# Kernel tuning notes

Measured on AMD Instinct MI355X. Metric: run time of the kernel, lower is better.

The kernel has to match this reference:

```python
import jax, jax.numpy as jnp
import numpy as np

NUM_HEADS = 16
NUM_KV_HEADS = 4
ROPE_THETA = 10000.0


def apply_rope(x, position_ids, theta):
    # x: [B, S, h, d]; position_ids: [B, S]
    d = x.shape[-1]
    freqs = 1.0 / theta ** (jnp.arange(0, d, 2, dtype=jnp.float32) / d)  # [d/2]
    angles = position_ids.astype(jnp.float32)[..., None] * freqs          # [B, S, d/2]
    cos = jnp.cos(angles)[:, :, None, :]                                  # [B, S, 1, d/2]
    sin = jnp.sin(angles)[:, :, None, :]
    xr = x.astype(jnp.float32).reshape(*x.shape[:-1], d // 2, 2)
    x0, x1 = xr[..., 0], xr[..., 1]
    o0 = x0 * cos - x1 * sin
    o1 = x0 * sin + x1 * cos
    out = jnp.stack((o0, o1), axis=-1).reshape(*x.shape)
    return out.astype(x.dtype)


def setup_inputs() -> dict:
    key = jax.random.key(0)
    k0, k1, k2, k3, k4 = jax.random.split(key, 5)
    B, S, H = 1, 2048, 2048
    Hkv = H // (NUM_HEADS // NUM_KV_HEADS)  # 512
    init_scale = 0.02 / np.sqrt(H)
    return {
        "hidden_states": jax.random.normal(k0, (B, S, H), jnp.float32),
        "attention_mask": jnp.ones((B, S), jnp.int32),
        "segment_ids": jnp.zeros((B, S), jnp.int32),
        "position_ids": jnp.broadcast_to(jnp.arange(S, dtype=jnp.int32)[None], (B, S)),
        "Wq": jax.random.normal(k1, (H, H), jnp.float32) * init_scale,
        "Wk": jax.random.normal(k2, (H, Hkv), jnp.float32) * init_scale,
        "Wv": jax.random.normal(k3, (H, Hkv), jnp.float32) * init_scale,
        "Wo": jax.random.normal(k4, (H, H), jnp.float32) * init_scale,
    }


def reference(hidden_states, attention_mask, segment_ids, position_ids, Wq, Wk, Wv, Wo):
    B, S, H = hidden_states.shape
    nh, nkv = NUM_HEADS, NUM_KV_HEADS
    g = nh // nkv
    hd = H // nh

    xq = (hidden_states @ Wq).reshape(B, S, nh, hd)
    xk = (hidden_states @ Wk).reshape(B, S, nkv, hd)
    xv = (hidden_states @ Wv).reshape(B, S, nkv, hd)
    # GQA repeat: 'b s (h d) -> b s (h g) d' == repeat each kv head g times contiguously
    xk = jnp.repeat(xk, g, axis=2)  # [B, S, nh, hd]
    xv = jnp.repeat(xv, g, axis=2)

    xq = apply_rope(xq, position_ids, ROPE_THETA)
    xk = apply_rope(xk, position_ids, ROPE_THETA)

    # masks: causal AND padding AND segment
    causal = jnp.tril(jnp.ones((S, S), dtype=bool))[None, None]            # [1,1,S,S]
    pad = (attention_mask > 0)[:, None, None, :]                            # [B,1,1,S]
    seg = (segment_ids[:, :, None] == segment_ids[:, None, :])[:, None]     # [B,1,S,S]
    mask = causal & pad & seg                                               # [B,1,S,S]

    scale = 1.0 / np.sqrt(hd)
    logits = jnp.einsum("bqhd,bkhd->bhqk", xq.astype(jnp.float32), xk.astype(jnp.float32)) * scale
    logits = jnp.where(mask, logits, jnp.finfo(jnp.float32).min)
    probs = jax.nn.softmax(logits, axis=-1).astype(xv.dtype)
    attn = jnp.einsum("bhqk,bkhd->bqhd", probs, xv)                         # [B,S,nh,hd]

    out = attn.reshape(B, S, H) @ Wo
    return out
```

## Files before the change

kernel.cpp:

```cpp
#include <hip/hip_runtime.h>
#include <hip/hip_bf16.h>
#include <stdint.h>
#include <math.h>

#define SS 2048
#define HH 2048
#define NH 16
#define NKV 4
#define HD 128
#define HKV 512
#define NQKV 3072

typedef __bf16 bf16x8 __attribute__((ext_vector_type(8)));
typedef float f32x4 __attribute__((ext_vector_type(4)));

static_assert(sizeof(bf16x8) == 16, "bf16x8 must be 16B");

__device__ __forceinline__ void async_ld16(const void* gp, void* lp) {
  __builtin_amdgcn_global_load_lds(
      (const __attribute__((address_space(1))) unsigned int*)(uintptr_t)gp,
      (__attribute__((address_space(3))) unsigned int*)(uintptr_t)lp,
      16, 0, 0);
}

__device__ __forceinline__ unsigned short f2bu(float f) {
  __hip_bfloat16 b = __float2bfloat16(f);
  return *reinterpret_cast<unsigned short*>(&b);
}

__global__ __launch_bounds__(256) void k_prep1(
    const float* __restrict__ X, const float* __restrict__ Wq, const float* __restrict__ Wk,
    const float* __restrict__ Wv, const float* __restrict__ Wo,
    const int* __restrict__ amv, const int* __restrict__ seg, int* __restrict__ kseg,
    float2* __restrict__ rtab, float* __restrict__ Obuf,
    __hip_bfloat16* __restrict__ Xb, __hip_bfloat16* __restrict__ WqT,
    __hip_bfloat16* __restrict__ WkT, __hip_bfloat16* __restrict__ WvT,
    __hip_bfloat16* __restrict__ WoT) {
  __shared__ __align__(16) __hip_bfloat16 t2[64 * 72];
  int b = blockIdx.x;
  int t = threadIdx.y * 32 + threadIdx.x;
  if (b < 4096) {
    int i = b * 256 + t;
    float4 v = ((const float4*)X)[i];
    ushort4 o;
    o.x = f2bu(v.x); o.y = f2bu(v.y); o.z = f2bu(v.z); o.w = f2bu(v.w);
    ((ushort4*)Xb)[i] = o;
    return;
  }
  b -= 4096;
  if (b >= 3080) {
    int i = (b - 3080) * 256 + t;
    ((float4*)Obuf)[i] = make_float4(0.f, 0.f, 0.f, 0.f);
    return;
  }
  if (b >= 2568) {
    int i = (b - 2568) * 256 + t;
    int p = i >> 6, f = i & 63;
    const float L2T_D64 = 0.20762050593046837f;
    float freq = exp2f(-L2T_D64 * (float)f);
    float sn, cs;
    sincosf((float)p * freq, &sn, &cs);
    rtab[i] = make_float2(sn, cs);
    return;
  }
  if (b >= 2560) {
    int i = (b - 2560) * 256 + t;
    kseg[i] = (amv[i] > 0) ? seg[i] : 0x7fffffff;
    return;
  }
  const float* src; __hip_bfloat16* dst; int xtiles;
  if (b < 1024)      { src = Wq; dst = WqT; xtiles = 32; }
  else if (b < 2048) { src = Wo; dst = WoT; xtiles = 32; b -= 1024; }
  else if (b < 2304) { src = Wk; dst = WkT; xtiles = 8;  b -= 2048; }
  else               { src = Wv; dst = WvT; xtiles = 8;  b -= 2304; }
  const int C = xtiles * 64;
  int bx = (b % xtiles) * 64;
  int by = (b / xtiles) * 64;
#pragma unroll
  for (int i = 0; i < 4; i++) {
    int idx = i * 256 + t;
    int r = idx >> 4, c4 = (idx & 15) * 4;
    float4 v = *(const float4*)(src + (size_t)(by + r) * C + bx + c4);
    t2[(c4 + 0) * 72 + r] = __float2bfloat16(v.x);
    t2[(c4 + 1) * 72 + r] = __float2bfloat16(v.y);
    t2[(c4 + 2) * 72 + r] = __float2bfloat16(v.z);
    t2[(c4 + 3) * 72 + r] = __float2bfloat16(v.w);
  }
  __syncthreads();
#pragma unroll
  for (int i = 0; i < 2; i++) {
    int idx = i * 256 + t;
    int rr = idx >> 3, cc = (idx & 7) * 8;
    *(bf16x8*)(dst + (size_t)(bx + rr) * HH + by + cc) =
        *(const bf16x8*)(&t2[rr * 72 + cc]);
  }
}

__global__ __launch_bounds__(256, 2) void k_gemm_qkv(
    const __hip_bfloat16* __restrict__ A, const __hip_bfloat16* __restrict__ B,
    __hip_bfloat16* __restrict__ Qb, __hip_bfloat16* __restrict__ Kb,
    __hip_bfloat16* __restrict__ Vt, const int* __restrict__ pos,
    const float2* __restrict__ rtab) {
  __shared__ __align__(16) __hip_bfloat16 sA[2][128 * 64];
  __shared__ __align__(16) __hip_bfloat16 sB[2][96 * 64];
  const int tid = threadIdx.x;
  const int lane = tid & 63;
  const int wave = tid >> 6;
  const int lid = blockIdx.x;
  const int xcd = lid & 7;
  const int idx = lid >> 3;
  const int bm = ((xcd & 3) * 4 + (idx & 3)) * 128;
  const int bn = ((xcd >> 2) * 16 + (idx >> 2)) * 96;
  const int wm = (wave & 1) * 64;
  const int wn = (wave >> 1) * 48;
  const int am = lane & 15;
  const int ch = lane >> 4;

  f32x4 acc[4][3] = {};

  auto stage = [&](int p, int k0) {
#pragma unroll
    for (int q = 0; q < 4; q++) {
      int c = q * 256 + tid;
      int row = c >> 3, kp = c & 7;
      int col = (kp ^ (row & 7)) * 8;
      async_ld16(A + (size_t)(bm + row) * HH + k0 + col, (char*)&sA[p][0] + c * 16);
    }
#pragma unroll
    for (int q = 0; q < 3; q++) {
      int c = q * 256 + tid;
      int row = c >> 3, kp = c & 7;
      int col = (kp ^ (row & 7)) * 8;
      async_ld16(B + (size_t)(bn + row) * HH + k0 + col, (char*)&sB[p][0] + c * 16);
    }
  };
  auto compute = [&](int p) {
#pragma unroll
    for (int kb = 0; kb < 2; kb++) {
      bf16x8 a[4], b[3];
#pragma unroll
      for (int i = 0; i < 4; i++) {
        int row = wm + i * 16 + am;
        a[i] = *(const bf16x8*)(&sA[p][0] + row * 64 + (((kb * 4 + ch) ^ (row & 7)) * 8));
      }
#pragma unroll
      for (int j = 0; j < 3; j++) {
        int row = wn + j * 16 + am;
        b[j] = *(const bf16x8*)(&sB[p][0] + row * 64 + (((kb * 4 + ch) ^ (row & 7)) * 8));
      }
#pragma unroll
      for (int i = 0; i < 4; i++)
#pragma unroll
        for (int j = 0; j < 3; j++)
          acc[i][j] = __builtin_amdgcn_mfma_f32_16x16x32_bf16(a[i], b[j], acc[i][j], 0, 0, 0);
    }
  };

  stage(0, 0);
  int cur = 0;
  for (int t = 0; t < 32; ++t) {
    if (t + 1 < 32) {
      stage(cur ^ 1, (t + 1) * 64);
      asm volatile("s_waitcnt vmcnt(7)" ::: "memory");
    } else {
      asm volatile("s_waitcnt vmcnt(0)" ::: "memory");
    }
    asm volatile("s_barrier" ::: "memory");
    compute(cur);
    asm volatile("s_barrier" ::: "memory");
    cur ^= 1;
  }

  const float SCLQ = 0.08838834764831845f * 1.4426950408889634f;
  const float sgn = (am & 1) ? 1.0f : -1.0f;
  int pint[4][4];
#pragma unroll
  for (int i = 0; i < 4; i++)
#pragma unroll
    for (int r = 0; r < 4; r++)
      pint[i][r] = pos[bm + wm + i * 16 + ch * 4 + r];
#pragma unroll
  for (int j = 0; j < 3; j++) {
    const int colbase = bn + wn + j * 16;
    const int col = colbase + am;
    if (colbase >= HH + HKV) {
      int lc = col - (HH + HKV);
#pragma unroll
      for (int i = 0; i < 4; i++) {
        int row = bm + wm + i * 16 + ch * 4;
        ushort4 o;
        o.x = f2bu(acc[i][j][0]); o.y = f2bu(acc[i][j][1]);
        o.z = f2bu(acc[i][j][2]); o.w = f2bu(acc[i][j][3]);
        *(ushort4*)(Vt + (size_t)lc * SS + row) = o;
      }
    } else {
      const bool isQ = (colbase < HH);
      int lc = isQ ? col : (col - HH);
      int fidx = (lc >> 1) & 63;
#pragma unroll
      for (int i = 0; i < 4; i++)
#pragma unroll
        for (int r = 0; r < 4; r++) {
          float v = acc[i][j][r];
          float px = __shfl_xor(v, 1, 64);
          float2 sc = rtab[pint[i][r] * 64 + fidx];
          float o = v * sc.y + sgn * px * sc.x;
          int row = bm + wm + i * 16 + ch * 4 + r;
          if (isQ) Qb[(size_t)row * HH + col] = __float2bfloat16(o * SCLQ);
          else     Kb[(size_t)row * HKV + lc] = __float2bfloat16(o);
        }
    }
  }
}

__global__ __launch_bounds__(256, 3) void k_gemm_out(
    const __hip_bfloat16* __restrict__ A, const __hip_bfloat16* __restrict__ B,
    float* __restrict__ C) {
  __shared__ __align__(16) __hip_bfloat16 sA0[64 * 64];
  __shared__ __align__(16) __hip_bfloat16 sB0[128 * 64];
  __shared__ __align__(16) __hip_bfloat16 sA1[64 * 64];
  __shared__ __align__(16) __hip_bfloat16 sB1[128 * 64];
  const int tid = threadIdx.x;
  const int lane = tid & 63;
  const int wave = tid >> 6;
  const int bm = blockIdx.y * 64;
  const int bn = blockIdx.x * 128;
  const int wm = (wave & 1) * 32;
  const int wn = (wave >> 1) * 64;
  const int am = lane & 15;
  const int ch = lane >> 4;

  f32x4 acc[2][4] = {};

  auto stage = [&](__hip_bfloat16* sA, __hip_bfloat16* sB, int k0) {
#pragma unroll
    for (int q = 0; q < 2; q++) {
      int c = q * 256 + tid;
      int row = c >> 3, kp = c & 7;
      int col = (kp ^ (row & 7)) * 8;
      async_ld16(A + (size_t)(bm + row) * HH + k0 + col, (char*)sA + c * 16);
    }
#pragma unroll
    for (int q = 0; q < 4; q++) {
      int c = q * 256 + tid;
      int row = c >> 3, kp = c & 7;
      int col = (kp ^ (row & 7)) * 8;
      async_ld16(B + (size_t)(bn + row) * HH + k0 + col, (char*)sB + c * 16);
    }
  };
  auto compute = [&](const __hip_bfloat16* sA, const __hip_bfloat16* sB) {
#pragma unroll
    for (int kb = 0; kb < 2; kb++) {
      bf16x8 a[2], b[4];
#pragma unroll
      for (int i = 0; i < 2; i++) {
        int row = wm + i * 16 + am;
        a[i] = *(const bf16x8*)(sA + row * 64 + (((kb * 4 + ch) ^ (row & 7)) * 8));
      }
#pragma unroll
      for (int j = 0; j < 4; j++) {
        int row = wn + j * 16 + am;
        b[j] = *(const bf16x8*)(sB + row * 64 + (((kb * 4 + ch) ^ (row & 7)) * 8));
      }
#pragma unroll
      for (int i = 0; i < 2; i++)
#pragma unroll
        for (int j = 0; j < 4; j++)
          acc[i][j] = __builtin_amdgcn_mfma_f32_16x16x32_bf16(a[i], b[j], acc[i][j], 0, 0, 0);
    }
  };

  stage(sA0, sB0, 0);
  int k0 = 0;
  while (true) {
    __syncthreads();
    if (k0 + 64 < HH) stage(sA1, sB1, k0 + 64);
    compute(sA0, sB0);
    k0 += 64; if (k0 >= HH) break;
    __syncthreads();
    if (k0 + 64 < HH) stage(sA0, sB0, k0 + 64);
    compute(sA1, sB1);
    k0 += 64; if (k0 >= HH) break;
  }

#pragma unroll
  for (int i = 0; i < 2; i++)
#pragma unroll
    for (int j = 0; j < 4; j++)
#pragma unroll
      for (int r = 0; r < 4; r++) {
        int row = bm + wm + i * 16 + ch * 4 + r;
        int col = bn + wn + j * 16 + am;
        C[(size_t)row * HH + col] = acc[i][j][r];
      }
}

__global__ __launch_bounds__(256, 4) void k_attn(
    const __hip_bfloat16* __restrict__ Qb,
    const __hip_bfloat16* __restrict__ Kb,
    const __hip_bfloat16* __restrict__ Vt,
    const int* __restrict__ seg,
    const int* __restrict__ kseg,
    float* __restrict__ Obuf,
    float* __restrict__ Lbuf) {
  __shared__ __align__(16) __hip_bfloat16 sK[2][32 * 128];
  __shared__ __align__(16) __hip_bfloat16 sV[2][128 * 32];
  __shared__ __align__(16) __hip_bfloat16 sPall[4][16 * 32];

  const int bid = blockIdx.x;
  const int r4 = bid >> 8;
  const int s = (bid & 255) >> 3;
  const int t4 = bid & 7;
  int qtb = (r4 & 2) ? ((s + 16) & 31) : s;
  const int qt = (r4 & 1) ? (31 - qtb) : qtb;
  const int h = (t4 >> 1) * 4 + r4;
  const int half = t4 & 1;
  const int T = 2 * (qt + 1);
  const int n0 = qt + 1;
  const int kt0 = half ? n0 : 0;
  const int kt1 = half ? T : n0;

  const int kvh = h >> 2;
  const int tid = threadIdx.x, lane = tid & 63, w = tid >> 6;
  const int am = lane & 15, ch = lane >> 4;
  const int qrow0 = qt * 64 + w * 16;
  char* sP = (char*)&sPall[w][0];

  bf16x8 qf[4];
#pragma unroll
  for (int ks = 0; ks < 4; ks++)
    qf[ks] = *(const bf16x8*)(Qb + (size_t)(qrow0 + am) * HH + h * HD + ks * 32 + ch * 8);

  int segq[4];
#pragma unroll
  for (int r = 0; r < 4; r++) segq[r] = seg[qrow0 + ch * 4 + r];
  const int q0 = seg[qrow0];
  const bool quni = __all((segq[0] == q0) && (segq[1] == q0) &&
                          (segq[2] == q0) && (segq[3] == q0));

  f32x4 o_acc[8] = {};
  float l_s[4] = {0.f, 0.f, 0.f, 0.f};

  auto stage = [&](int kt, int p) {
#pragma unroll
    for (int q = 0; q < 2; q++) {
      int c = q * 256 + tid;
      int row = c >> 4, kp = c & 15;
      int col = (kp ^ (row & 15)) * 8;
      async_ld16(Kb + (size_t)(kt * 32 + row) * HKV + kvh * 128 + col, (char*)sK[p] + c * 16);
    }
#pragma unroll
    for (int q = 0; q < 2; q++) {
      int c = q * 256 + tid;
      int row = c >> 2, kp = c & 3;
      int col = (kp ^ ((row >> 1) & 3)) * 8;
      async_ld16(Vt + (size_t)(kvh * 128 + row) * SS + kt * 32 + col, (char*)sV[p] + c * 16);
    }
  };

  stage(kt0, 0);
  for (int kt = kt0; kt < kt1; kt++) {
    const int p = (kt - kt0) & 1;
    const int kbase = kt * 32;
    const bool skip = (kbase > qrow0 + 15);
    __syncthreads();

    int kinfo[2];
    if (!skip) {
#pragma unroll
      for (int jt = 0; jt < 2; jt++) kinfo[jt] = kseg[kbase + jt * 16 + am];
    }
    if (kt + 1 < kt1) stage(kt + 1, p ^ 1);
    if (!skip) {
      f32x4 sacc[2] = {};
      __builtin_amdgcn_s_setprio(1);
#pragma unroll
      for (int ks = 0; ks < 4; ks++)
#pragma unroll
        for (int jt = 0; jt < 2; jt++) {
          bf16x8 kf = *(const bf16x8*)(sK[p] + (jt * 16 + am) * 128 + (((ks * 4 + ch) ^ am) * 8));
          sacc[jt] = __builtin_amdgcn_mfma_f32_16x16x32_bf16(qf[ks], kf, sacc[jt], 0, 0, 0);
        }
      __builtin_amdgcn_s_setprio(0);

      const bool needc = (kbase + 31 > qrow0);
      const bool fast = quni && !needc &&
          __all((kinfo[0] == q0) && (kinfo[1] == q0));

      if (fast) {
#pragma unroll
        for (int jt = 0; jt < 2; jt++)
#pragma unroll
          for (int r = 0; r < 4; r++) {
            float pv = exp2f(sacc[jt][r] - 8.0f);
            l_s[r] += pv;
            int row = ch * 4 + r;
            int chunk = (jt * 2 + (am >> 3)) ^ ch;
            *(__hip_bfloat16*)(sP + row * 64 + chunk * 16 + (am & 7) * 2) =
                __float2bfloat16(pv);
          }
      } else {
#pragma unroll
        for (int jt = 0; jt < 2; jt++) {
          int kk = kbase + jt * 16 + am;
#pragma unroll
          for (int r = 0; r < 4; r++) {
            int qrow = qrow0 + ch * 4 + r;
            bool ok = (kinfo[jt] == segq[r]) && (kk <= qrow);
            float pv = ok ? exp2f(sacc[jt][r] - 8.0f) : 0.0f;
            l_s[r] += pv;
            int row = ch * 4 + r;
            int chunk = (jt * 2 + (am >> 3)) ^ ch;
            *(__hip_bfloat16*)(sP + row * 64 + chunk * 16 + (am & 7) * 2) =
                __float2bfloat16(pv);
          }
        }
      }

      __builtin_amdgcn_s_setprio(1);
      {
        bf16x8 pf = *(const bf16x8*)(sP + am * 64 + ((ch ^ ((am >> 2) & 3)) * 16));
#pragma unroll
        for (int jt = 0; jt < 8; jt++) {
          int vrow = jt * 16 + am;
          bf16x8 vf = *(const bf16x8*)(sV[p] + vrow * 32 + ((ch ^ ((vrow >> 1) & 3)) * 8));
          o_acc[jt] = __builtin_amdgcn_mfma_f32_16x16x32_bf16(pf, vf, o_acc[jt], 0, 0, 0);
        }
      }
      __builtin_amdgcn_s_setprio(0);
    }
  }

#pragma unroll
  for (int off = 1; off < 16; off <<= 1)
#pragma unroll
    for (int r = 0; r < 4; r++) l_s[r] += __shfl_xor(l_s[r], off, 64);
  if (am == 0)
#pragma unroll
    for (int r = 0; r < 4; r++)
      unsafeAtomicAdd(Lbuf + (size_t)(qrow0 + ch * 4 + r) * NH + h, l_s[r]);
#pragma unroll
  for (int jt = 0; jt < 8; jt++)
#pragma unroll
    for (int r = 0; r < 4; r++) {
      int row = qrow0 + ch * 4 + r;
      unsafeAtomicAdd(Obuf + (size_t)row * HH + h * HD + jt * 16 + am, o_acc[jt][r]);
    }
}

__global__ __launch_bounds__(256) void k_norm(
    const float* __restrict__ Obuf, const float* __restrict__ Lbuf,
    __hip_bfloat16* __restrict__ Ab) {
  int i = blockIdx.x * 256 + threadIdx.x;
  int s = i >> 9;
  int hIdx = (i & 511) >> 5;
  float inv = 1.0f / Lbuf[(size_t)s * NH + hIdx];
  float4 v = ((const float4*)Obuf)[i];
  ushort4 o;
  o.x = f2bu(v.x * inv); o.y = f2bu(v.y * inv);
  o.z = f2bu(v.z * inv); o.w = f2bu(v.w * inv);
  ((ushort4*)Ab)[i] = o;
}

extern "C" void kernel_launch(void* const* d_in, const int* in_sizes, int n_in,
                              void* d_out, int out_size, void* d_ws, size_t ws_size,
                              hipStream_t stream) {
  const float* X  = (const float*)d_in[0];
  const int* amv  = (const int*)d_in[1];
  const int* seg  = (const int*)d_in[2];
  const int* pos  = (const int*)d_in[3];
  const float* Wq = (const float*)d_in[4];
  const float* Wk = (const float*)d_in[5];
  const float* Wv = (const float*)d_in[6];
  const float* Wo = (const float*)d_in[7];
  float* out = (float*)d_out;

  char* ws = (char*)d_ws;
  size_t off = 0;
  auto alloc = [&](size_t bytes) { void* p = ws + off; off += (bytes + 255) & ~(size_t)255; return p; };
  __hip_bfloat16* Xb   = (__hip_bfloat16*)alloc((size_t)SS * HH * 2);
  __hip_bfloat16* WqT  = (__hip_bfloat16*)alloc((size_t)HH * HH * 2);
  __hip_bfloat16* WkT  = (__hip_bfloat16*)alloc((size_t)HKV * HH * 2);
  __hip_bfloat16* WvT  = (__hip_bfloat16*)alloc((size_t)HKV * HH * 2);
  __hip_bfloat16* WoT  = (__hip_bfloat16*)alloc((size_t)HH * HH * 2);
  __hip_bfloat16* Qb   = (__hip_bfloat16*)alloc((size_t)SS * HH * 2);
  __hip_bfloat16* Kb   = (__hip_bfloat16*)alloc((size_t)SS * HKV * 2);
  __hip_bfloat16* Vt   = (__hip_bfloat16*)alloc((size_t)HKV * SS * 2);
  float*          Obuf = (float*)alloc((size_t)SS * HH * 4);
  float*          Lbuf = (float*)alloc((size_t)SS * NH * 4);
  __hip_bfloat16* Ab   = (__hip_bfloat16*)alloc((size_t)SS * HH * 2);
  int*            kseg = (int*)alloc((size_t)SS * 4);
  float2*         rtab = (float2*)alloc((size_t)SS * 64 * 8);
  (void)WkT; (void)WvT;

  k_prep1<<<dim3(11304), dim3(32, 8), 0, stream>>>(X, Wq, Wk, Wv, Wo, amv, seg, kseg,
                                                   rtab, Obuf, Xb, WqT, WkT, WvT, WoT);
  k_gemm_qkv<<<dim3(512), 256, 0, stream>>>(Xb, WqT, Qb, Kb, Vt, pos, rtab);
  k_attn<<<dim3(1024), 256, 0, stream>>>(Qb, Kb, Vt, seg, kseg, Obuf, Lbuf);
  k_norm<<<dim3(SS * HH / 4 / 256), 256, 0, stream>>>(Obuf, Lbuf, Ab);
  k_gemm_out<<<dim3(HH / 128, SS / 64), 256, 0, stream>>>(Ab, WoT, out);
}
```

Before: 215.1 us.

## Distribute independent prep work into tail blocks of QKV GEMM and attention kernels

The Obuf/Lbuf zeroing and the kseg mask computation move from the prep kernel into extra blocks appended to the QKV GEMM launch. The Wo transpose-to-bf16 moves into extra blocks appended to the attention launch, reusing the sK shared buffer. The aim is to shrink the memory-bound prep kernel and let this independent work fill idle CUs during the compute-bound kernels' tail waves. The cost is larger grids and added branch logic, and the extra blocks may compete for bandwidth or occupancy with the main blocks.

```diff
diff --git a/kernel.cpp b/kernel.cpp
--- a/kernel.cpp
+++ b/kernel.cpp
@@ -30,12 +30,9 @@
 
 __global__ __launch_bounds__(256) void k_prep1(
     const float* __restrict__ X, const float* __restrict__ Wq, const float* __restrict__ Wk,
-    const float* __restrict__ Wv, const float* __restrict__ Wo,
-    const int* __restrict__ amv, const int* __restrict__ seg, int* __restrict__ kseg,
-    float2* __restrict__ rtab, float* __restrict__ Obuf,
+    const float* __restrict__ Wv, float2* __restrict__ rtab,
     __hip_bfloat16* __restrict__ Xb, __hip_bfloat16* __restrict__ WqT,
-    __hip_bfloat16* __restrict__ WkT, __hip_bfloat16* __restrict__ WvT,
-    __hip_bfloat16* __restrict__ WoT) {
+    __hip_bfloat16* __restrict__ WkT, __hip_bfloat16* __restrict__ WvT) {
   __shared__ __align__(16) __hip_bfloat16 t2[64 * 72];
   int b = blockIdx.x;
   int t = threadIdx.y * 32 + threadIdx.x;
@@ -48,13 +45,8 @@
     return;
   }
   b -= 4096;
-  if (b >= 3080) {
-    int i = (b - 3080) * 256 + t;
-    ((float4*)Obuf)[i] = make_float4(0.f, 0.f, 0.f, 0.f);
-    return;
-  }
-  if (b >= 2568) {
-    int i = (b - 2568) * 256 + t;
+  if (b >= 1536) {
+    int i = (b - 1536) * 256 + t;
     int p = i >> 6, f = i & 63;
     const float L2T_D64 = 0.20762050593046837f;
     float freq = exp2f(-L2T_D64 * (float)f);
@@ -63,16 +55,10 @@
     rtab[i] = make_float2(sn, cs);
     return;
   }
-  if (b >= 2560) {
-    int i = (b - 2560) * 256 + t;
-    kseg[i] = (amv[i] > 0) ? seg[i] : 0x7fffffff;
-    return;
-  }
   const float* src; __hip_bfloat16* dst; int xtiles;
   if (b < 1024)      { src = Wq; dst = WqT; xtiles = 32; }
-  else if (b < 2048) { src = Wo; dst = WoT; xtiles = 32; b -= 1024; }
-  else if (b < 2304) { src = Wk; dst = WkT; xtiles = 8;  b -= 2048; }
-  else               { src = Wv; dst = WvT; xtiles = 8;  b -= 2304; }
+  else if (b < 1280) { src = Wk; dst = WkT; xtiles = 8;  b -= 1024; }
+  else               { src = Wv; dst = WvT; xtiles = 8;  b -= 1280; }
   const int C = xtiles * 64;
   int bx = (b % xtiles) * 64;
   int by = (b / xtiles) * 64;
@@ -100,13 +86,25 @@
     const __hip_bfloat16* __restrict__ A, const __hip_bfloat16* __restrict__ B,
     __hip_bfloat16* __restrict__ Qb, __hip_bfloat16* __restrict__ Kb,
     __hip_bfloat16* __restrict__ Vt, const int* __restrict__ pos,
-    const float2* __restrict__ rtab) {
+    const float2* __restrict__ rtab, float* __restrict__ Obuf,
+    const int* __restrict__ amv, const int* __restrict__ seg,
+    int* __restrict__ kseg) {
   __shared__ __align__(16) __hip_bfloat16 sA[2][128 * 64];
   __shared__ __align__(16) __hip_bfloat16 sB[2][96 * 64];
   const int tid = threadIdx.x;
+  const int lid = blockIdx.x;
+  if (lid >= 512) {
+    int j = lid - 512;
+    if (j < 4128) {
+      ((float4*)Obuf)[j * 256 + tid] = make_float4(0.f, 0.f, 0.f, 0.f);
+    } else {
+      int i = (j - 4128) * 256 + tid;
+      kseg[i] = (amv[i] > 0) ? seg[i] : 0x7fffffff;
+    }
+    return;
+  }
   const int lane = tid & 63;
   const int wave = tid >> 6;
-  const int lid = blockIdx.x;
   const int xcd = lid & 7;
   const int idx = lid >> 3;
   const int bm = ((xcd & 3) * 4 + (idx & 3)) * 128;
@@ -302,12 +300,42 @@
     const int* __restrict__ seg,
     const int* __restrict__ kseg,
     float* __restrict__ Obuf,
-    float* __restrict__ Lbuf) {
+    float* __restrict__ Lbuf,
+    const float* __restrict__ Wo,
+    __hip_bfloat16* __restrict__ WoT) {
   __shared__ __align__(16) __hip_bfloat16 sK[2][32 * 128];
   __shared__ __align__(16) __hip_bfloat16 sV[2][128 * 32];
   __shared__ __align__(16) __hip_bfloat16 sPall[4][16 * 32];
 
   const int bid = blockIdx.x;
+  const int tid = threadIdx.x;
+
+  if (bid >= 1024) {
+    __hip_bfloat16* t2 = &sK[0][0];
+    int b = bid - 1024;
+    int bx = (b & 31) * 64;
+    int by = (b >> 5) * 64;
+#pragma unroll
+    for (int i = 0; i < 4; i++) {
+      int idx = i * 256 + tid;
+      int r = idx >> 4, c4 = (idx & 15) * 4;
+      float4 v = *(const float4*)(Wo + (size_t)(by + r) * HH + bx + c4);
+      t2[(c4 + 0) * 72 + r] = __float2bfloat16(v.x);
+      t2[(c4 + 1) * 72 + r] = __float2bfloat16(v.y);
+      t2[(c4 + 2) * 72 + r] = __float2bfloat16(v.z);
+      t2[(c4 + 3) * 72 + r] = __float2bfloat16(v.w);
+    }
+    __syncthreads();
+#pragma unroll
+    for (int i = 0; i < 2; i++) {
+      int idx = i * 256 + tid;
+      int rr = idx >> 3, cc = (idx & 7) * 8;
+      *(bf16x8*)(WoT + (size_t)(bx + rr) * HH + by + cc) =
+          *(const bf16x8*)(&t2[rr * 72 + cc]);
+    }
+    return;
+  }
+
   const int r4 = bid >> 8;
   const int s = (bid & 255) >> 3;
   const int t4 = bid & 7;
@@ -321,7 +349,7 @@
   const int kt1 = half ? T : n0;
 
   const int kvh = h >> 2;
-  const int tid = threadIdx.x, lane = tid & 63, w = tid >> 6;
+  const int lane = tid & 63, w = tid >> 6;
   const int am = lane & 15, ch = lane >> 4;
   const int qrow0 = qt * 64 + w * 16;
   char* sP = (char*)&sPall[w][0];
@@ -493,10 +521,11 @@
   float2*         rtab = (float2*)alloc((size_t)SS * 64 * 8);
   (void)WkT; (void)WvT;
 
-  k_prep1<<<dim3(11304), dim3(32, 8), 0, stream>>>(X, Wq, Wk, Wv, Wo, amv, seg, kseg,
-                                                   rtab, Obuf, Xb, WqT, WkT, WvT, WoT);
-  k_gemm_qkv<<<dim3(512), 256, 0, stream>>>(Xb, WqT, Qb, Kb, Vt, pos, rtab);
-  k_attn<<<dim3(1024), 256, 0, stream>>>(Qb, Kb, Vt, seg, kseg, Obuf, Lbuf);
+  k_prep1<<<dim3(6144), dim3(32, 8), 0, stream>>>(X, Wq, Wk, Wv, rtab,
+                                                  Xb, WqT, WkT, WvT);
+  k_gemm_qkv<<<dim3(4648), 256, 0, stream>>>(Xb, WqT, Qb, Kb, Vt, pos, rtab,
+                                             Obuf, amv, seg, kseg);
+  k_attn<<<dim3(2048), 256, 0, stream>>>(Qb, Kb, Vt, seg, kseg, Obuf, Lbuf, Wo, WoT);
   k_norm<<<dim3(SS * HH / 4 / 256), 256, 0, stream>>>(Obuf, Lbuf, Ab);
   k_gemm_out<<<dim3(HH / 128, SS / 64), 256, 0, stream>>>(Ab, WoT, out);
 }
```

New measurement: 215.5 us (median of 2 runs). Within noise of the previous version (+0.2%).
